# Performance work log

Measured on AMD Instinct MI355X. Metric: run time of the kernel, lower is better.

Reference implementation:

```python
import jax, jax.numpy as jnp
import numpy as np

# --- CSV_Architecture_v2 layout (mediapipe hands: 21 landmarks per hand) ---
INTRO = np.arange(0, 3)                 # vector_intro_idxs
H0_IDX, H0_PROB = 3, 4                  # handedness_0_idx, handedness_0_prob_idx
HAND0_X = np.arange(5, 26)
HAND0_Y = np.arange(26, 47)
HAND0_Z = np.arange(47, 68)
H1_IDX, H1_PROB = 68, 69
HAND1_X = np.arange(70, 91)
HAND1_Y = np.arange(91, 112)
HAND1_Z = np.arange(112, 133)
FRAME_REPR_LEN = 133
NO_HAND = -1.0                          # arch.no_hand_detected_val

B, S = 256, 2048


def setup_inputs() -> dict:
    key = jax.random.key(0)
    k1, k2, k3 = jax.random.split(key, 3)
    X = jax.random.normal(k1, (B, S, FRAME_REPR_LEN), dtype=jnp.float32)
    h0 = jnp.where(jax.random.bernoulli(k2, 0.3, (B, S)), NO_HAND, 1.0)
    h1 = jnp.where(jax.random.bernoulli(k3, 0.3, (B, S)), NO_HAND, 1.0)
    X = X.at[:, :, H0_IDX].set(h0).at[:, :, H1_IDX].set(h1)
    return {"X": X}


def _hand_sub_matrix(x, hidx, xi, yi, zi):
    """x: [S, F]. Build the per-hand subtraction matrix of strategy 'seq_on_last':
    find the MOST RECENT frame where this hand is valid, take its wrist (x,y,z),
    and subtract that wrist from this hand's coord columns on every valid frame."""
    S = x.shape[0]
    valid = x[:, hidx] != NO_HAND                      # [S] bool
    any_valid = jnp.any(valid)
    t = jnp.arange(S)
    last = jnp.maximum(jnp.max(jnp.where(valid, t, -1)), 0)  # last valid frame (safe)
    wrist_cols = jnp.array([xi[0], yi[0], zi[0]])
    ref = x[last, wrist_cols]                          # [3] reference wrist
    sub_vec = (jnp.zeros((x.shape[1],), x.dtype)
               .at[xi].set(ref[0])
               .at[yi].set(ref[1])
               .at[zi].set(ref[2]))                    # [F]
    row_mask = (valid & any_valid).astype(x.dtype)     # subtract only on valid frames
    return row_mask[:, None] * sub_vec[None, :]        # [S, F]


def reference(X):
    """Strategy 'seq_on_last': per sequence, per hand, normalize coords to the
    most recent valid wrist point. Vectorized over batch (original: tf.map_fn)."""
    def per_seq(x):  # x: [S, F]
        s0 = _hand_sub_matrix(x, H0_IDX, HAND0_X, HAND0_Y, HAND0_Z)
        s1 = _hand_sub_matrix(x, H1_IDX, HAND1_X, HAND1_Y, HAND1_Z)
        return x - (s0 + s1)
    return jax.vmap(per_seq)(X)
```

## Files before the change

### kernel.cpp

```cpp
#include <hip/hip_runtime.h>

#define SEQ 2048
#define FR  133
#define H0I 3
#define H1I 68
#define NOHAND -1.0f

#define CH_FRAMES 256
#define CH_ELEMS  (CH_FRAMES * FR)
#define CH_VEC    (CH_ELEMS / 4)
#define CH_MAIN   ((CH_VEC / 1024) * 1024)
#define NCHUNK    (SEQ / CH_FRAMES)

typedef float f32x4 __attribute__((ext_vector_type(4)));

__global__ __launch_bounds__(64) void refs_kernel(
    const float* __restrict__ X, float* __restrict__ refs ) {
    const int b    = blockIdx.x;
    const int lane = threadIdx.x;
    const float* xb = X + (size_t)b * (SEQ * FR);

    int last0 = -1, last1 = -1;
    for (int start = SEQ - 64; ; start -= 64) {
        int t = start + lane;
        float v0 = xb[(size_t)t * FR + H0I];
        float v1 = xb[(size_t)t * FR + H1I];
        unsigned long long b0 = __ballot(v0 != NOHAND);
        unsigned long long b1 = __ballot(v1 != NOHAND);
        if (last0 < 0 && b0) last0 = start + 63 - __builtin_clzll(b0);
        if (last1 < 0 && b1) last1 = start + 63 - __builtin_clzll(b1);
        if ((last0 >= 0 && last1 >= 0) || start == 0) break;
    }
    if (lane == 0) {
        int l0 = last0 < 0 ? 0 : last0;
        int l1 = last1 < 0 ? 0 : last1;
        float* r = refs + b * 8;
        r[0] = xb[(size_t)l0 * FR + 5];
        r[1] = xb[(size_t)l0 * FR + 26];
        r[2] = xb[(size_t)l0 * FR + 47];
        r[3] = xb[(size_t)l1 * FR + 70];
        r[4] = xb[(size_t)l1 * FR + 91];
        r[5] = xb[(size_t)l1 * FR + 112];
    }
}

__device__ __forceinline__ float subval(int f, int mk,
    float r0x, float r0y, float r0z, float r1x, float r1y, float r1z) {
    float s0 = (f >= 47) ? r0z : ((f >= 26) ? r0y : r0x);
    float s1 = (f >= 112) ? r1z : ((f >= 91) ? r1y : r1x);
    bool h0 = (f >= 5) & (f < 68) & ((mk & 1) != 0);
    bool h1 = (f >= 70) & ((mk & 2) != 0);
    return h0 ? s0 : (h1 ? s1 : 0.0f);
}

__global__ __launch_bounds__(256) void stream_kernel(
    const float* __restrict__ X, float* __restrict__ Out,
    const float* __restrict__ refs) {
    __shared__ unsigned char s_mask[CH_FRAMES];
    __shared__ float s_ref[6];

    const int blk = blockIdx.x;
    const int seq = blk >> 3;
    const int ch  = blk & (NCHUNK - 1);
    const int tid = threadIdx.x;

    const float* xb = X   + (size_t)seq * (SEQ * FR) + (size_t)ch * CH_ELEMS;
    float*       ob = Out + (size_t)seq * (SEQ * FR) + (size_t)ch * CH_ELEMS;

    {
        float v0 = xb[(size_t)tid * FR + H0I];
        float v1 = xb[(size_t)tid * FR + H1I];
        s_mask[tid] = (unsigned char)((v0 != NOHAND) | ((v1 != NOHAND) << 1));
    }
    if (tid < 6) s_ref[tid] = refs[seq * 8 + tid];
    __syncthreads();

    const float r0x = s_ref[0], r0y = s_ref[1], r0z = s_ref[2];
    const float r1x = s_ref[3], r1y = s_ref[4], r1z = s_ref[5];

    const f32x4* xv = (const f32x4*)xb;
    f32x4*       ov = (f32x4*)ob;

    auto process = [&](f32x4& v, int i) {
        int e     = i * 4;
        int frame = (int)((unsigned)e / 133u);
        int f0    = e - frame * 133;
        #pragma unroll
        for (int j = 0; j < 4; ++j) {
            int f = f0 + j, fr = frame;
            if (f >= FR) { f -= FR; fr += 1; }
            int mk = s_mask[fr];
            v[j] -= subval(f, mk, r0x, r0y, r0z, r1x, r1y, r1z);
        }
    };

    for (int base = tid; base + 768 < CH_VEC; base += 1024) {
        f32x4 v[4];
        #pragma unroll
        for (int u = 0; u < 4; ++u) v[u] = xv[base + u * 256];
        #pragma unroll
        for (int u = 0; u < 4; ++u) {
            int i = base + u * 256;
            process(v[u], i);
            __builtin_nontemporal_store(v[u], &ov[i]);
        }
    }
    for (int i = CH_MAIN + tid; i < CH_VEC; i += 256) {
        f32x4 v = xv[i];
        process(v, i);
        __builtin_nontemporal_store(v, &ov[i]);
    }
}

extern "C" void kernel_launch(void* const* d_in, const int* in_sizes, int n_in,
                              void* d_out, int out_size, void* d_ws, size_t ws_size,
                              hipStream_t stream) {
    const float* X = (const float*)d_in[0];
    float* Out     = (float*)d_out;
    float* refs    = (float*)d_ws;
    int nB = in_sizes[0] / (SEQ * FR);
    refs_kernel<<<nB, 64, 0, stream>>>(X, refs);
    stream_kernel<<<nB * NCHUNK, 256, 0, stream>>>(X, Out, refs);
}
```

Baseline: 119.7 us.

## Fuse reference-wrist search into streaming kernel and deepen load batching

Drops the separate refs_kernel. Each streaming block now finds the last valid frame of its sequence itself, first with a 256-frame tail scan spread over all four waves, then with a serial fallback scan when needed, and loads the reference wrists into shared memory. This removes one kernel launch and the dependency between the two kernels. In exchange, all 8 chunk blocks of a sequence redo the same tail search, which adds extra strided loads before streaming starts. The main loop also issues 8 vector loads per thread instead of 4, and launch bounds now request 8 blocks per SM.

```diff
diff --git a/kernel.cpp b/kernel.cpp
--- a/kernel.cpp
+++ b/kernel.cpp
@@ -9,40 +9,12 @@
 #define CH_FRAMES 256
 #define CH_ELEMS  (CH_FRAMES * FR)
 #define CH_VEC    (CH_ELEMS / 4)
-#define CH_MAIN   ((CH_VEC / 1024) * 1024)
 #define NCHUNK    (SEQ / CH_FRAMES)
+#define DEPTH     8
+#define CH_MAIN   ((CH_VEC / (DEPTH * 256)) * (DEPTH * 256))
+#define TAILW     256
 
 typedef float f32x4 __attribute__((ext_vector_type(4)));
-
-__global__ __launch_bounds__(64) void refs_kernel(
-    const float* __restrict__ X, float* __restrict__ refs ) {
-    const int b    = blockIdx.x;
-    const int lane = threadIdx.x;
-    const float* xb = X + (size_t)b * (SEQ * FR);
-
-    int last0 = -1, last1 = -1;
-    for (int start = SEQ - 64; ; start -= 64) {
-        int t = start + lane;
-        float v0 = xb[(size_t)t * FR + H0I];
-        float v1 = xb[(size_t)t * FR + H1I];
-        unsigned long long b0 = __ballot(v0 != NOHAND);
-        unsigned long long b1 = __ballot(v1 != NOHAND);
-        if (last0 < 0 && b0) last0 = start + 63 - __builtin_clzll(b0);
-        if (last1 < 0 && b1) last1 = start + 63 - __builtin_clzll(b1);
-        if ((last0 >= 0 && last1 >= 0) || start == 0) break;
-    }
-    if (lane == 0) {
-        int l0 = last0 < 0 ? 0 : last0;
-        int l1 = last1 < 0 ? 0 : last1;
-        float* r = refs + b * 8;
-        r[0] = xb[(size_t)l0 * FR + 5];
-        r[1] = xb[(size_t)l0 * FR + 26];
-        r[2] = xb[(size_t)l0 * FR + 47];
-        r[3] = xb[(size_t)l1 * FR + 70];
-        r[4] = xb[(size_t)l1 * FR + 91];
-        r[5] = xb[(size_t)l1 * FR + 112];
-    }
-}
 
 __device__ __forceinline__ float subval(int f, int mk,
     float r0x, float r0y, float r0z, float r1x, float r1y, float r1z) {
@@ -53,26 +25,61 @@
     return h0 ? s0 : (h1 ? s1 : 0.0f);
 }
 
-__global__ __launch_bounds__(256) void stream_kernel(
-    const float* __restrict__ X, float* __restrict__ Out,
-    const float* __restrict__ refs) {
+__global__ __launch_bounds__(256, 8) void fused_kernel(
+    const float* __restrict__ X, float* __restrict__ Out) {
     __shared__ unsigned char s_mask[CH_FRAMES];
     __shared__ float s_ref[6];
+    __shared__ int s_last[2][4];
 
-    const int blk = blockIdx.x;
-    const int seq = blk >> 3;
-    const int ch  = blk & (NCHUNK - 1);
-    const int tid = threadIdx.x;
+    const int blk  = blockIdx.x;
+    const int seq  = blk >> 3;
+    const int ch   = blk & (NCHUNK - 1);
+    const int tid  = threadIdx.x;
+    const int wave = tid >> 6, lane = tid & 63;
 
-    const float* xb = X   + (size_t)seq * (SEQ * FR) + (size_t)ch * CH_ELEMS;
-    float*       ob = Out + (size_t)seq * (SEQ * FR) + (size_t)ch * CH_ELEMS;
+    const float* xseq = X + (size_t)seq * (SEQ * FR);
+    const float* xb   = xseq + (size_t)ch * CH_ELEMS;
+    float*       ob   = Out + (size_t)seq * (SEQ * FR) + (size_t)ch * CH_ELEMS;
 
-    {
-        float v0 = xb[(size_t)tid * FR + H0I];
-        float v1 = xb[(size_t)tid * FR + H1I];
-        s_mask[tid] = (unsigned char)((v0 != NOHAND) | ((v1 != NOHAND) << 1));
+    float m0v = xb[(size_t)tid * FR + H0I];
+    float m1v = xb[(size_t)tid * FR + H1I];
+    const int tf = SEQ - TAILW + tid;
+    float t0v = xseq[(size_t)tf * FR + H0I];
+    float t1v = xseq[(size_t)tf * FR + H1I];
+
+    s_mask[tid] = (unsigned char)((m0v != NOHAND) | ((m1v != NOHAND) << 1));
+    unsigned long long b0 = __ballot(t0v != NOHAND);
+    unsigned long long b1 = __ballot(t1v != NOHAND);
+    if (lane == 0) {
+        int base = SEQ - TAILW + wave * 64;
+        s_last[0][wave] = b0 ? (base + 63 - __builtin_clzll(b0)) : -1;
+        s_last[1][wave] = b1 ? (base + 63 - __builtin_clzll(b1)) : -1;
     }
-    if (tid < 6) s_ref[tid] = refs[seq * 8 + tid];
+    __syncthreads();
+
+    if (wave == 0) {
+        int l0 = max(max(s_last[0][0], s_last[0][1]), max(s_last[0][2], s_last[0][3]));
+        int l1 = max(max(s_last[1][0], s_last[1][1]), max(s_last[1][2], s_last[1][3]));
+        if ((l0 < 0) | (l1 < 0)) {
+            for (int start = SEQ - TAILW - 64; start >= 0; start -= 64) {
+                int t = start + lane;
+                float v0 = xseq[(size_t)t * FR + H0I];
+                float v1 = xseq[(size_t)t * FR + H1I];
+                unsigned long long c0 = __ballot(v0 != NOHAND);
+                unsigned long long c1 = __ballot(v1 != NOHAND);
+                if (l0 < 0 && c0) l0 = start + 63 - __builtin_clzll(c0);
+                if (l1 < 0 && c1) l1 = start + 63 - __builtin_clzll(c1);
+                if ((l0 >= 0) & (l1 >= 0)) break;
+            }
+            if (l0 < 0) l0 = 0;
+            if (l1 < 0) l1 = 0;
+        }
+        if (lane < 6) {
+            const int col[6] = {5, 26, 47, 70, 91, 112};
+            int fr = (lane < 3) ? l0 : l1;
+            s_ref[lane] = xseq[(size_t)fr * FR + col[lane]];
+        }
+    }
     __syncthreads();
 
     const float r0x = s_ref[0], r0y = s_ref[1], r0z = s_ref[2];
@@ -94,12 +101,12 @@
         }
     };
 
-    for (int base = tid; base + 768 < CH_VEC; base += 1024) {
-        f32x4 v[4];
+    for (int base = tid; base + (DEPTH - 1) * 256 < CH_VEC; base += DEPTH * 256) {
+        f32x4 v[DEPTH];
         #pragma unroll
-        for (int u = 0; u < 4; ++u) v[u] = xv[base + u * 256];
+        for (int u = 0; u < DEPTH; ++u) v[u] = xv[base + u * 256];
         #pragma unroll
-        for (int u = 0; u < 4; ++u) {
+        for (int u = 0; u < DEPTH; ++u) {
             int i = base + u * 256;
             process(v[u], i);
             __builtin_nontemporal_store(v[u], &ov[i]);
@@ -117,8 +124,6 @@
                               hipStream_t stream) {
     const float* X = (const float*)d_in[0];
     float* Out     = (float*)d_out;
-    float* refs    = (float*)d_ws;
     int nB = in_sizes[0] / (SEQ * FR);
-    refs_kernel<<<nB, 64, 0, stream>>>(X, refs);
-    stream_kernel<<<nB * NCHUNK, 256, 0, stream>>>(X, Out, refs);
+    fused_kernel<<<nB * NCHUNK, 256, 0, stream>>>(X, Out);
 }
```

Measured after the change: 136.4 us. 13.9% more time.
